# Performance work log

Measured on AMD Instinct MI355X. Metric: run time of the kernel, lower is better.

Reference implementation:

```python
import jax, jax.numpy as jnp
import numpy as np

HIDDEN = 1024
INTER = 256
N_EXPERTS = 16
B, T = 4, 2048
NEG_INF = -1000000000.0


def setup_inputs() -> dict:
    key = jax.random.key(0)
    ks = jax.random.split(key, 5)
    hidden_states = jax.random.normal(ks[0], (B, T, HIDDEN), dtype=jnp.float32)
    sim_matrix = jax.random.normal(ks[1], (HIDDEN, N_EXPERTS), dtype=jnp.float32)
    threshold = jnp.zeros((1,), dtype=jnp.float32)
    # torch Linear weights: w1 [I, C], w2 [C, I]; store per-expert stacked in
    # matmul-friendly layout: w1 [E, C, I], w2 [E, I, C]
    w1 = jax.random.normal(ks[2], (N_EXPERTS, HIDDEN, INTER), dtype=jnp.float32) / np.sqrt(HIDDEN)
    w2 = jax.random.normal(ks[3], (N_EXPERTS, INTER, HIDDEN), dtype=jnp.float32) / np.sqrt(INTER)
    return {"hidden_states": hidden_states, "sim_matrix": sim_matrix,
            "threshold": threshold, "w1": w1, "w2": w2}


def _l2norm(x, axis):
    return x / jnp.maximum(jnp.linalg.norm(x, axis=axis, keepdims=True), 1e-12)


def reference(hidden_states, sim_matrix, threshold, w1, w2):
    Bq, Tq, C = hidden_states.shape
    x = hidden_states.reshape(-1, C)                      # [N, C]
    # gate
    scores = _l2norm(x, -1) @ _l2norm(sim_matrix, 0)      # [N, E]
    activated = scores > threshold
    k_per_token = activated.sum(axis=-1)                  # [N] int
    masked = jnp.where(activated, scores, NEG_INF)
    routing_weights = jax.nn.softmax(masked, axis=-1)     # [N, E]
    # dense all-expert FFN
    h = jax.nn.gelu(jnp.einsum('nc,eci->nei', x, w1), approximate=False)
    out = jnp.einsum('nei,eic->nec', h, w2)               # [N, E, C]
    final = jnp.einsum('nec,ne->nc', out, routing_weights)
    return final.reshape(Bq, Tq, C), scores, k_per_token
```

## Files before the change

kernel.cpp:

```cpp
#include <hip/hip_runtime.h>
#include <hip/hip_bf16.h>
#include <math.h>

#define NTOK 8192
#define HID  1024
#define ISZ  256
#define NEXP 16
#define NBIG 4096

typedef __attribute__((ext_vector_type(8))) short bf16x8;
typedef __attribute__((ext_vector_type(4))) float f32x4;

#define MFMA16(a, b, c) __builtin_amdgcn_mfma_f32_16x16x32_bf16(a, b, c, 0, 0, 0)

__device__ __forceinline__ unsigned short f2bf(float f) {
  unsigned u = __float_as_uint(f);
  u += 0x7fff + ((u >> 16) & 1);
  return (unsigned short)(u >> 16);
}

__device__ __forceinline__ void async16(void* l, const void* g) {
  __builtin_amdgcn_global_load_lds(
      (const __attribute__((address_space(1))) unsigned int*)g,
      (__attribute__((address_space(3))) unsigned int*)l, 16, 0, 0);
}

__global__ void simnorm_kernel(const float* __restrict__ sm, float* __restrict__ inv_smn) {
  __shared__ float red[16][17];
  int t = threadIdx.x;
  int e = t & 15, g = t >> 4;
  float ss = 0.f;
  for (int c = g; c < HID; c += 16) {
    float v = sm[c * NEXP + e];
    ss += v * v;
  }
  red[e][g] = ss;
  __syncthreads();
  if (t < 16) {
    float s = 0.f;
    #pragma unroll
    for (int i = 0; i < 16; i++) s += red[t][i];
    inv_smn[t] = 1.f / fmaxf(sqrtf(s), 1e-12f);
  }
}

__global__ __launch_bounds__(256)
void gate_kernel(const float* __restrict__ x, const float* __restrict__ sm,
                 const float* __restrict__ thr, const float* __restrict__ inv_smn,
                 float* __restrict__ scores_out, float* __restrict__ k_out,
                 float* __restrict__ rw_out, unsigned short* __restrict__ xb_out) {
  const int n = blockIdx.x;
  const int t = threadIdx.x;
  const int lane = t & 63, wave = t >> 6;
  const float* xr = x + (size_t)n * HID;

  float p[16];
  #pragma unroll
  for (int e = 0; e < 16; e++) p[e] = 0.f;
  float ss = 0.f;

  #pragma unroll
  for (int q = 0; q < 4; q++) {
    int c = t + q * 256;
    float v = xr[c];
    ss += v * v;
    xb_out[(size_t)n * HID + c] = f2bf(v);
    const float4* smr = (const float4*)(sm + (size_t)c * NEXP);
    float4 s0 = smr[0], s1 = smr[1], s2 = smr[2], s3 = smr[3];
    p[0] += v * s0.x;  p[1] += v * s0.y;  p[2] += v * s0.z;  p[3] += v * s0.w;
    p[4] += v * s1.x;  p[5] += v * s1.y;  p[6] += v * s1.z;  p[7] += v * s1.w;
    p[8] += v * s2.x;  p[9] += v * s2.y;  p[10] += v * s2.z; p[11] += v * s2.w;
    p[12] += v * s3.x; p[13] += v * s3.y; p[14] += v * s3.z; p[15] += v * s3.w;
  }

  #pragma unroll
  for (int off = 32; off > 0; off >>= 1) {
    ss += __shfl_down(ss, off, 64);
    #pragma unroll
    for (int e = 0; e < 16; e++) p[e] += __shfl_down(p[e], off, 64);
  }

  __shared__ float red[4][17];
  __shared__ float sc[16];
  if (lane == 0) {
    red[wave][0] = ss;
    #pragma unroll
    for (int e = 0; e < 16; e++) red[wave][1 + e] = p[e];
  }
  __syncthreads();

  if (t < 16) {
    float d = red[0][1 + t] + red[1][1 + t] + red[2][1 + t] + red[3][1 + t];
    float ssum = red[0][0] + red[1][0] + red[2][0] + red[3][0];
    float inv_x = 1.f / fmaxf(sqrtf(ssum), 1e-12f);
    float s = d * inv_x * inv_smn[t];
    scores_out[(size_t)n * 16 + t] = s;
    sc[t] = s;
  }
  __syncthreads();

  if (t < 16) {
    float thrv = thr[0];
    float s = sc[t];
    bool act = s > thrv;
    float m = act ? s : -INFINITY;
    int cnt = act ? 1 : 0;
    #pragma unroll
    for (int off = 8; off > 0; off >>= 1) {
      m = fmaxf(m, __shfl_xor(m, off, 16));
      cnt += __shfl_xor(cnt, off, 16);
    }
    float pv;
    if (cnt > 0) pv = act ? expf(s - m) : 0.f;
    else         pv = 1.f;
    float sum = pv;
    #pragma unroll
    for (int off = 8; off > 0; off >>= 1) sum += __shfl_xor(sum, off, 16);
    rw_out[(size_t)n * 16 + t] = pv / sum;
    if (t == 0) k_out[n] = (float)cnt;
  }
}

__global__ __launch_bounds__(256)
void transpose_cast_kernel(const float* __restrict__ src, unsigned short* __restrict__ dst,
                           int R, int C, int dstride, int e_src_stride, int e_dst_mult) {
  __shared__ float tile[32][33];
  const int e = blockIdx.z;
  const int r0 = blockIdx.y * 32, c0 = blockIdx.x * 32;
  const int tx = threadIdx.x & 31, ty = threadIdx.x >> 5;
  const float* s = src + (size_t)e * e_src_stride;
  #pragma unroll
  for (int q = 0; q < 4; q++) {
    int r = r0 + ty + q * 8;
    tile[ty + q * 8][tx] = s[(size_t)r * C + c0 + tx];
  }
  __syncthreads();
  unsigned short* d = dst + (size_t)e * e_dst_mult;
  #pragma unroll
  for (int q = 0; q < 4; q++) {
    int cc = c0 + ty + q * 8;
    int r  = r0 + tx;
    d[(size_t)cc * dstride + r] = f2bf(tile[tx][ty + q * 8]);
  }
}

#define GTILE(CA, CB, NA, NB, kn)                                                     \
  {                                                                                   \
    _Pragma("unroll")                                                                 \
    for (int i = 0; i < 2; i++) {                                                     \
      async16((NA) + o16[i],         Ag + (size_t)aRow[i] * LD + (kn) + aCol[i]);     \
      async16((NB) + o16[i],         Bg + (size_t)bRow[i] * LD + (kn) + bCol[i]);     \
      async16((NA) + 16384 + o16[i], Ag + (size_t)(aRow[i] + 64) * LD + (kn) + aCol[i]); \
      async16((NB) + 16384 + o16[i], Bg + (size_t)(bRow[i] + 32) * LD + (kn) + bCol[i]); \
    }                                                                                 \
    _Pragma("unroll")                                                                 \
    for (int kk = 0; kk < 2; kk++) {                                                  \
      const int ck = kk ? colk1 : colk0;                                              \
      bf16x8 a[8], b[4];                                                              \
      _Pragma("unroll")                                                               \
      for (int q = 0; q < 2; q++)                                                     \
        _Pragma("unroll")                                                             \
        for (int ml = 0; ml < 4; ml++)                                                \
          a[q * 4 + ml] = *(const bf16x8*)((CA) + q * 16384 + wmo + ml * 2048 + lro + ck); \
      _Pragma("unroll")                                                               \
      for (int qn = 0; qn < 2; qn++)                                                  \
        _Pragma("unroll")                                                             \
        for (int nl = 0; nl < 2; nl++)                                                \
          b[qn * 2 + nl] = *(const bf16x8*)((CB) + qn * 16384 + wno + nl * 2048 + lro + ck); \
      _Pragma("unroll")                                                               \
      for (int m8 = 0; m8 < 8; m8++)                                                  \
        _Pragma("unroll")                                                             \
        for (int n4 = 0; n4 < 4; n4++)                                                \
          acc[m8][n4] = MFMA16(a[m8], b[n4], acc[m8][n4]);                            \
    }                                                                                 \
    __builtin_amdgcn_sched_barrier(0);                                                \
    asm volatile("s_waitcnt vmcnt(0)" ::: "memory");                                  \
    __builtin_amdgcn_s_barrier();                                                     \
    __builtin_amdgcn_sched_barrier(0);                                                \
  }

template <int EPI, int KEXT, int LD, int NBN, int SPLITK>
__global__ __launch_bounds__(512, 2)
void gemm256(const unsigned short* __restrict__ A, const unsigned short* __restrict__ B,
             float* __restrict__ Cf, float* __restrict__ Cf2,
             unsigned short* __restrict__ Cb, const float* __restrict__ rw) {
  __shared__ __align__(1024) char lds[131072];
  constexpr int NT = KEXT / 64;
  const int tid = threadIdx.x;
  const int lane = tid & 63, wid = tid >> 6;
  const int wm = wid >> 2, wn = wid & 3;
  const int lr = lane & 15;

  const int nwg = gridDim.x;
  const int cpx = nwg >> 3;
  int wg = (blockIdx.x & 7) * cpx + (blockIdx.x >> 3);
  int kz = 0;
  if (SPLITK == 2) { kz = wg / (nwg >> 1); wg = wg % (nwg >> 1); }
  const int bm = wg / NBN, bn = wg % NBN;

  const int swz = (lr & 7) << 4;
  const int colk0 = ((lane >> 4) * 16) ^ swz;
  const int colk1 = (64 + (lane >> 4) * 16) ^ swz;
  const int wmo = wm * 8192, wno = wn * 4096, lro = lr * 128;

  int aRow[2], aCol[2], bRow[2], bCol[2], o16[2];
  #pragma unroll
  for (int i = 0; i < 2; i++) {
    int o = (i * 512 + tid) * 16;
    o16[i] = o;
    { int wmb = o >> 13, ob = o & 8191, r = ob >> 7, cb = ob & 127;
      aRow[i] = wmb * 128 + r; aCol[i] = (cb ^ ((r & 7) << 4)) >> 1; }
    { int wnb = o >> 12, ob = o & 4095, r = ob >> 7, cb = ob & 127;
      bRow[i] = wnb * 64 + r; bCol[i] = (cb ^ ((r & 7) << 4)) >> 1; }
  }

  const unsigned short* Ag = A + (size_t)bm * 256 * LD + (size_t)kz * KEXT;
  const unsigned short* Bg = B + (size_t)bn * 256 * LD + (size_t)kz * KEXT;

  f32x4 acc[8][4];
  #pragma unroll
  for (int m = 0; m < 8; m++)
    #pragma unroll
    for (int n = 0; n < 4; n++) acc[m][n] = (f32x4){0.f, 0.f, 0.f, 0.f};

  #pragma unroll
  for (int i = 0; i < 2; i++) {
    async16(lds + o16[i],                 Ag + (size_t)aRow[i] * LD + aCol[i]);
    async16(lds + 65536 + o16[i],         Bg + (size_t)bRow[i] * LD + bCol[i]);
    async16(lds + 16384 + o16[i],         Ag + (size_t)(aRow[i] + 64) * LD + aCol[i]);
    async16(lds + 65536 + 16384 + o16[i], Bg + (size_t)(bRow[i] + 32) * LD + bCol[i]);
  }
  asm volatile("s_waitcnt vmcnt(0)" ::: "memory");
  __builtin_amdgcn_s_barrier();
  __builtin_amdgcn_sched_barrier(0);

  #pragma unroll 1
  for (int t = 0; t < NT; t += 2) {
    GTILE(lds,         lds + 65536,         lds + 32768, lds + 65536 + 32768,
          ((t + 1) & (NT - 1)) << 6)
    GTILE(lds + 32768, lds + 65536 + 32768, lds,         lds + 65536,
          ((t + 2) & (NT - 1)) << 6)
  }

  asm volatile("s_waitcnt vmcnt(0)" ::: "memory");

  const int jr = (lane >> 4) * 4;
  if (EPI == 1) {
    float wrow[8][4];
    #pragma unroll
    for (int m = 0; m < 8; m++)
      #pragma unroll
      for (int j = 0; j < 4; j++)
        wrow[m][j] = rw[(size_t)(bm * 256 + wm * 128 + m * 16 + jr + j) * 16 + bn];
    #pragma unroll
    for (int m = 0; m < 8; m++) {
      #pragma unroll
      for (int n = 0; n < 4; n++) {
        int col = bn * 256 + wn * 64 + n * 16 + lr;
        #pragma unroll
        for (int j = 0; j < 4; j++) {
          int r = bm * 256 + wm * 128 + m * 16 + jr + j;
          float v = acc[m][n][j];
          float g = 0.7978845608f * (v + 0.044715f * v * v * v);
          float e = __expf(2.f * g);
          float th = 1.f - 2.f / (e + 1.f);
          float ge = 0.5f * v * (1.f + th);
          Cb[(size_t)r * NBIG + col] = f2bf(ge * wrow[m][j]);
        }
      }
    }
  } else {
    float* cfp = (SPLITK == 2 && kz == 1) ? Cf2 : Cf;
    #pragma unroll
    for (int m = 0; m < 8; m++) {
      #pragma unroll
      for (int n = 0; n < 4; n++) {
        int col = bn * 256 + wn * 64 + n * 16 + lr;
        #pragma unroll
        for (int j = 0; j < 4; j++) {
          int r = bm * 256 + wm * 128 + m * 16 + jr + j;
          cfp[(size_t)r * HID + col] = acc[m][n][j];
        }
      }
    }
  }
}

__global__ __launch_bounds__(256)
void addk(float* __restrict__ out, const float* __restrict__ p1, int n4) {
  int i = blockIdx.x * blockDim.x + threadIdx.x;
  const int stride = gridDim.x * blockDim.x;
  for (; i < n4; i += stride) {
    float4 a = ((const float4*)out)[i];
    float4 b = ((const float4*)p1)[i];
    a.x += b.x; a.y += b.y; a.z += b.z; a.w += b.w;
    ((float4*)out)[i] = a;
  }
}

extern "C" void kernel_launch(void* const* d_in, const int* in_sizes, int n_in,
                              void* d_out, int out_size, void* d_ws, size_t ws_size,
                              hipStream_t stream) {
  const float* x   = (const float*)d_in[0];
  const float* sm  = (const float*)d_in[1];
  const float* thr = (const float*)d_in[2];
  const float* w1  = (const float*)d_in[3];
  const float* w2  = (const float*)d_in[4];

  float* out_final  = (float*)d_out;
  float* out_scores = out_final + (size_t)NTOK * HID;
  float* out_k      = out_scores + (size_t)NTOK * NEXP;

  char* ws = (char*)d_ws;
  size_t off = 0;
  float* inv_smn = (float*)(ws + off); off += 256;
  float* rwbuf   = (float*)(ws + off); off += (size_t)NTOK * NEXP * 4;
  unsigned short* Xb  = (unsigned short*)(ws + off); off += (size_t)NTOK * HID * 2;
  unsigned short* W1T = (unsigned short*)(ws + off); off += (size_t)NBIG * HID * 2;
  unsigned short* W2T = (unsigned short*)(ws + off); off += (size_t)HID * NBIG * 2;
  unsigned short* H   = (unsigned short*)(ws + off); off += (size_t)NTOK * NBIG * 2;
  float* P1 = (float*)(ws + off);
  const bool split = ws_size >= off + (size_t)NTOK * HID * 4;

  simnorm_kernel<<<1, 256, 0, stream>>>(sm, inv_smn);
  gate_kernel<<<NTOK, 256, 0, stream>>>(x, sm, thr, inv_smn, out_scores, out_k, rwbuf, Xb);
  transpose_cast_kernel<<<dim3(ISZ / 32, HID / 32, NEXP), 256, 0, stream>>>(
      w1, W1T, HID, ISZ, HID, HID * ISZ, ISZ * HID);
  transpose_cast_kernel<<<dim3(HID / 32, ISZ / 32, NEXP), 256, 0, stream>>>(
      w2, W2T, ISZ, HID, NBIG, ISZ * HID, ISZ);

  gemm256<1, HID, HID, 16, 1><<<512, 512, 0, stream>>>(Xb, W1T, nullptr, nullptr, H, rwbuf);

  if (split) {
    gemm256<2, NBIG / 2, NBIG, 4, 2><<<256, 512, 0, stream>>>(H, W2T, out_final, P1, nullptr, nullptr);
    addk<<<2048, 256, 0, stream>>>(out_final, P1, NTOK * HID / 4);
  } else {
    gemm256<2, NBIG, NBIG, 4, 1><<<128, 512, 0, stream>>>(H, W2T, out_final, nullptr, nullptr, nullptr);
  }
}
```

Before: 235.8 us.

## Split GEMM tile loop into quarter phases with staggered async loads

Each 64-wide k-step is broken into four sub-tile phases over A and B quadrants. Async global-to-LDS loads for the next buffers are issued piecemeal in individual phases, and partial vmcnt waits replace full drains, so memory traffic overlaps MFMA work at finer granularity. s_setprio is raised around the MFMA clusters. This adds more barriers per tile and relies on tricky quadrant-level buffer reuse ordering, which risks races and extra sync overhead.

```diff
diff --git a/kernel.cpp b/kernel.cpp
--- a/kernel.cpp
+++ b/kernel.cpp
@@ -144,37 +144,44 @@
   }
 }
 
-#define GTILE(CA, CB, NA, NB, kn)                                                     \
+#define SU_A0(dst, kn) { async16((dst) + o16[0], Ag + (size_t)aRow[0] * LD + (kn) + aCol[0]); \
+                         async16((dst) + o16[1], Ag + (size_t)aRow[1] * LD + (kn) + aCol[1]); }
+#define SU_A1(dst, kn) { async16((dst) + 16384 + o16[0], Ag + (size_t)(aRow[0] + 64) * LD + (kn) + aCol[0]); \
+                         async16((dst) + 16384 + o16[1], Ag + (size_t)(aRow[1] + 64) * LD + (kn) + aCol[1]); }
+#define SU_B0(dst, kn) { async16((dst) + o16[0], Bg + (size_t)bRow[0] * LD + (kn) + bCol[0]); \
+                         async16((dst) + o16[1], Bg + (size_t)bRow[1] * LD + (kn) + bCol[1]); }
+#define SU_B1(dst, kn) { async16((dst) + 16384 + o16[0], Bg + (size_t)(bRow[0] + 32) * LD + (kn) + bCol[0]); \
+                         async16((dst) + 16384 + o16[1], Bg + (size_t)(bRow[1] + 32) * LD + (kn) + bCol[1]); }
+
+#define PHZ(QM, QN, bA, bB, WAITV, ...)                                               \
   {                                                                                   \
+    bf16x8 afr[4][2], bfr[2][2];                                                      \
     _Pragma("unroll")                                                                 \
-    for (int i = 0; i < 2; i++) {                                                     \
-      async16((NA) + o16[i],         Ag + (size_t)aRow[i] * LD + (kn) + aCol[i]);     \
-      async16((NB) + o16[i],         Bg + (size_t)bRow[i] * LD + (kn) + bCol[i]);     \
-      async16((NA) + 16384 + o16[i], Ag + (size_t)(aRow[i] + 64) * LD + (kn) + aCol[i]); \
-      async16((NB) + 16384 + o16[i], Bg + (size_t)(bRow[i] + 32) * LD + (kn) + bCol[i]); \
+    for (int ml = 0; ml < 4; ml++) {                                                  \
+      afr[ml][0] = *(const bf16x8*)((bA) + (QM)*16384 + wmo + ml*2048 + lro + colk0); \
+      afr[ml][1] = *(const bf16x8*)((bA) + (QM)*16384 + wmo + ml*2048 + lro + colk1); \
     }                                                                                 \
     _Pragma("unroll")                                                                 \
-    for (int kk = 0; kk < 2; kk++) {                                                  \
-      const int ck = kk ? colk1 : colk0;                                              \
-      bf16x8 a[8], b[4];                                                              \
+    for (int nl = 0; nl < 2; nl++) {                                                  \
+      bfr[nl][0] = *(const bf16x8*)((bB) + (QN)*16384 + wno + nl*2048 + lro + colk0); \
+      bfr[nl][1] = *(const bf16x8*)((bB) + (QN)*16384 + wno + nl*2048 + lro + colk1); \
+    }                                                                                 \
+    __VA_ARGS__                                                                       \
+    __builtin_amdgcn_sched_barrier(0);                                                \
+    __builtin_amdgcn_s_barrier();                                                     \
+    asm volatile("s_waitcnt lgkmcnt(0)" ::: "memory");                                \
+    __builtin_amdgcn_sched_barrier(0);                                                \
+    __builtin_amdgcn_s_setprio(1);                                                    \
+    _Pragma("unroll")                                                                 \
+    for (int ml = 0; ml < 4; ml++)                                                    \
       _Pragma("unroll")                                                               \
-      for (int q = 0; q < 2; q++)                                                     \
-        _Pragma("unroll")                                                             \
-        for (int ml = 0; ml < 4; ml++)                                                \
-          a[q * 4 + ml] = *(const bf16x8*)((CA) + q * 16384 + wmo + ml * 2048 + lro + ck); \
-      _Pragma("unroll")                                                               \
-      for (int qn = 0; qn < 2; qn++)                                                  \
-        _Pragma("unroll")                                                             \
-        for (int nl = 0; nl < 2; nl++)                                                \
-          b[qn * 2 + nl] = *(const bf16x8*)((CB) + qn * 16384 + wno + nl * 2048 + lro + ck); \
-      _Pragma("unroll")                                                               \
-      for (int m8 = 0; m8 < 8; m8++)                                                  \
-        _Pragma("unroll")                                                             \
-        for (int n4 = 0; n4 < 4; n4++)                                                \
-          acc[m8][n4] = MFMA16(a[m8], b[n4], acc[m8][n4]);                            \
-    }                                                                                 \
+      for (int nl = 0; nl < 2; nl++) {                                                \
+        acc[(QM)*4+ml][(QN)*2+nl] = MFMA16(afr[ml][0], bfr[nl][0], acc[(QM)*4+ml][(QN)*2+nl]); \
+        acc[(QM)*4+ml][(QN)*2+nl] = MFMA16(afr[ml][1], bfr[nl][1], acc[(QM)*4+ml][(QN)*2+nl]); \
+      }                                                                               \
+    __builtin_amdgcn_s_setprio(0);                                                    \
     __builtin_amdgcn_sched_barrier(0);                                                \
-    asm volatile("s_waitcnt vmcnt(0)" ::: "memory");                                  \
+    if (WAITV) { asm volatile("s_waitcnt vmcnt(4)" ::: "memory"); }                   \
     __builtin_amdgcn_s_barrier();                                                     \
     __builtin_amdgcn_sched_barrier(0);                                                \
   }
@@ -223,23 +230,34 @@
     #pragma unroll
     for (int n = 0; n < 4; n++) acc[m][n] = (f32x4){0.f, 0.f, 0.f, 0.f};
 
-  #pragma unroll
-  for (int i = 0; i < 2; i++) {
-    async16(lds + o16[i],                 Ag + (size_t)aRow[i] * LD + aCol[i]);
-    async16(lds + 65536 + o16[i],         Bg + (size_t)bRow[i] * LD + bCol[i]);
-    async16(lds + 16384 + o16[i],         Ag + (size_t)(aRow[i] + 64) * LD + aCol[i]);
-    async16(lds + 65536 + 16384 + o16[i], Bg + (size_t)(bRow[i] + 32) * LD + bCol[i]);
-  }
-  asm volatile("s_waitcnt vmcnt(0)" ::: "memory");
+  char* const b0A = lds;
+  char* const b1A = lds + 32768;
+  char* const b0B = lds + 65536;
+  char* const b1B = lds + 98304;
+
+  SU_A0(b0A, 0)
+  SU_B0(b0B, 0)
+  SU_A1(b0A, 0)
+  SU_B1(b0B, 0)
+  SU_A0(b1A, 64)
+  SU_B1(b1B, 64)
+  asm volatile("s_waitcnt vmcnt(4)" ::: "memory");
   __builtin_amdgcn_s_barrier();
   __builtin_amdgcn_sched_barrier(0);
 
   #pragma unroll 1
   for (int t = 0; t < NT; t += 2) {
-    GTILE(lds,         lds + 65536,         lds + 32768, lds + 65536 + 32768,
-          ((t + 1) & (NT - 1)) << 6)
-    GTILE(lds + 32768, lds + 65536 + 32768, lds,         lds + 65536,
-          ((t + 2) & (NT - 1)) << 6)
+    const int kn1 = ((t + 1) & (NT - 1)) << 6;
+    const int kn2 = ((t + 2) & (NT - 1)) << 6;
+    const int kn3 = ((t + 3) & (NT - 1)) << 6;
+    PHZ(0, 0, b0A, b0B, 0, SU_B0(b1B, kn1) SU_A1(b1A, kn1))
+    PHZ(0, 1, b0A, b0B, 0, )
+    PHZ(1, 1, b0A, b0B, 0, SU_A0(b0A, kn2))
+    PHZ(1, 0, b0A, b0B, 1, SU_B1(b0B, kn2))
+    PHZ(0, 0, b1A, b1B, 0, SU_B0(b0B, kn2) SU_A1(b0A, kn2))
+    PHZ(0, 1, b1A, b1B, 0, )
+    PHZ(1, 1, b1A, b1B, 0, SU_A0(b1A, kn3))
+    PHZ(1, 0, b1A, b1B, 1, SU_B1(b1B, kn3))
   }
 
   asm volatile("s_waitcnt vmcnt(0)" ::: "memory");
```

Result: slower. 243.2 us (+3.1%).
